# Kernel optimization log

Hardware: AMD Instinct MI355X
Metric: run time of the kernel (lower is better)

## Reference

```python
import jax, jax.numpy as jnp
import numpy as np

INSIZE = 1024
OUTSIZE = 1024
N_U = 20
N_V = 20
SIGMA_MIN = 0.6
SIGMA_MAX = 1.0
R = (SIGMA_MAX - SIGMA_MIN) / 2.0
SIGMA_MEAN = SIGMA_MIN + R
BATCH = 32768


def setup_inputs() -> dict:
    key = jax.random.key(0)
    k_x, k_U, k_p, k_V = jax.random.split(key, 4)
    x = jax.random.normal(k_x, (BATCH, INSIZE), dtype=jnp.float32)
    U = jnp.triu(jax.random.normal(k_U, (INSIZE, INSIZE), dtype=jnp.float32))
    V = jnp.triu(jax.random.normal(k_V, (OUTSIZE, OUTSIZE), dtype=jnp.float32))
    nsigma = min(INSIZE, OUTSIZE)
    p = 0.001 * jax.random.normal(k_p, (nsigma,), dtype=jnp.float32)
    bias = jnp.zeros((OUTSIZE,), dtype=jnp.float32)
    return {"x": x, "U": U, "p": p, "V": V, "bias": bias}


def _hprod(x, u, k):
    # x: [bs, dim], u: [dim], k static int. Householder reflection on the trailing k coords.
    xs = x[:, -k:]                     # [bs, k]
    us = u[-k:]                        # [k]
    alpha = 2.0 * (xs @ us) / jnp.sum(us * us)   # [bs]
    xs_new = xs - alpha[:, None] * us[None, :]
    if k < x.shape[1]:
        return jnp.concatenate([x[:, :-k], xs_new], axis=1)
    return xs_new


def _sigma_matrix(p):
    sigmas = 2.0 * R * (jax.nn.sigmoid(p) - 0.5) + SIGMA_MEAN   # [nsigma]
    nsigma = p.shape[0]
    S = jnp.zeros((INSIZE, OUTSIZE), dtype=p.dtype)
    idx = jnp.arange(nsigma)
    return S.at[idx, idx].set(sigmas)


def reference(x, U, p, V, bias):
    # U multiply: reflectors 0..N_U-1 with k = insize - i
    for i in range(N_U):
        x = _hprod(x, U[i], INSIZE - i)
    x = x @ _sigma_matrix(p)
    # V multiply: reflectors N_V-1..0 with k = outsize - i
    for i in range(N_V - 1, -1, -1):
        x = _hprod(x, V[i], OUTSIZE - i)
    return x + bias
```

## Files before the change

### kernel.cpp

```cpp
#include <hip/hip_runtime.h>
#include <hip/hip_bf16.h>

typedef __attribute__((ext_vector_type(8))) short bf16x8;
typedef __attribute__((ext_vector_type(4))) short bf16x4;
typedef __attribute__((ext_vector_type(4))) float f32x4;

#define NU 20

__device__ __forceinline__ float b2f(unsigned short u) {
    union { float f; unsigned v; } x; x.v = ((unsigned)u) << 16; return x.f;
}
__device__ __forceinline__ unsigned short f2b(float f) {
    union { float f; unsigned v; } x; x.f = f;
    unsigned r = x.v + 0x7FFF + ((x.v >> 16) & 1);
    return (unsigned short)(r >> 16);
}


__global__ __launch_bounds__(256) void k_gram(
        const float* __restrict__ U, const float* __restrict__ p,
        const float* __restrict__ V, const float* __restrict__ bias,
        float* __restrict__ GU, float* __restrict__ GV,
        float* __restrict__ s_ws, float* __restrict__ b_ws) {
    const int b = blockIdx.x, T = threadIdx.x;
    if (b >= 420) {
        int t = (b - 420) * 256 + T;
        float pv = p[t];
        s_ws[t] = 0.4f / (1.0f + __expf(-pv)) + 0.6f;
        b_ws[t] = bias[t];
        return;
    }
    const float* M = (b < 210) ? U : V;
    float* Gm = (b < 210) ? GU : GV;
    int i = (b < 210) ? b : b - 210;
    int k = 0;
    while ((k + 1) * (k + 2) / 2 <= i) k++;
    int j = i - k * (k + 1) / 2;
    f32x4 a4 = *(const f32x4*)&M[j * 1024 + T * 4];
    f32x4 b4 = *(const f32x4*)&M[k * 1024 + T * 4];
    float acc = a4[0] * b4[0] + a4[1] * b4[1] + a4[2] * b4[2] + a4[3] * b4[3];
    for (int off = 32; off; off >>= 1) acc += __shfl_down(acc, off, 64);
    __shared__ float part[4];
    if ((T & 63) == 0) part[T >> 6] = acc;
    __syncthreads();
    if (T == 0) {
        float s = part[0] + part[1] + part[2] + part[3];
        Gm[j * 20 + k] = s; Gm[k * 20 + j] = s;
    }
}

__global__ __launch_bounds__(256) void k_recur(
        const float* __restrict__ U, const float* __restrict__ V,
        const float* __restrict__ GUg, const float* __restrict__ GVg,
        const float* __restrict__ s_ws,
        float* __restrict__ A, float* __restrict__ Csc,
        unsigned short* __restrict__ Ft, unsigned short* __restrict__ G) {
    __shared__ float sGU[400], sGV[400];
    const int T = threadIdx.x;
    const int t = blockIdx.x * 256 + T;
    for (int i = T; i < 400; i += 256) { sGU[i] = GUg[i]; sGV[i] = GVg[i]; }
    __syncthreads();
    float sig = s_ws[t];
    float a[NU], c[NU];
    for (int k = 0; k < NU; k++) {
        float w = U[k * 1024 + t];
        for (int j = 0; j < k; j++) w -= a[j] * sGU[j * 20 + k];
        a[k] = (2.0f / sGU[k * 20 + k]) * w;
    }
    for (int k = NU - 1; k >= 0; k--) {
        float w = V[k * 1024 + t];
        for (int j = k + 1; j < NU; j++) w -= c[j] * sGV[j * 20 + k];
        c[k] = (2.0f / sGV[k * 20 + k]) * w;
    }
    for (int k = 0; k < NU; k++) { A[k * 1024 + t] = a[k]; Ft[k * 1024 + t] = f2b(a[k]); }
    for (int b = 0; b < NU; b++) Csc[b * 1024 + t] = sig * c[b];
    for (int k = 2 * NU; k < 64; k++) Ft[k * 1024 + t] = 0;
    for (int k = 0; k < NU; k++) G[t * 64 + k] = f2b(sig * U[k * 1024 + t]);
    for (int k = 0; k < NU; k++) G[t * 64 + NU + k] = f2b(V[k * 1024 + t]);
    for (int k = 2 * NU; k < 64; k++) G[t * 64 + k] = 0;
}

__global__ __launch_bounds__(256) void k_e(
        const float* __restrict__ U, const float* __restrict__ Csc,
        float* __restrict__ E) {
    const int aa = blockIdx.x / 20, bb = blockIdx.x % 20;
    const int T = threadIdx.x;
    f32x4 a4 = *(const f32x4*)&U[aa * 1024 + T * 4];
    f32x4 b4 = *(const f32x4*)&Csc[bb * 1024 + T * 4];
    float acc = a4[0] * b4[0] + a4[1] * b4[1] + a4[2] * b4[2] + a4[3] * b4[3];
    for (int off = 32; off; off >>= 1) acc += __shfl_down(acc, off, 64);
    __shared__ float part[4];
    if ((T & 63) == 0) part[T >> 6] = acc;
    __syncthreads();
    if (T == 0) E[aa * 20 + bb] = part[0] + part[1] + part[2] + part[3];
}

__global__ __launch_bounds__(256) void k_f2(
        const float* __restrict__ A, const float* __restrict__ Csc,
        const float* __restrict__ Eg, unsigned short* __restrict__ Ft) {
    __shared__ float sE[400];
    const int T = threadIdx.x;
    const int t = blockIdx.x * 256 + T;
    for (int i = T; i < 400; i += 256) sE[i] = Eg[i];
    __syncthreads();
    float av[NU];
    for (int a = 0; a < NU; a++) av[a] = A[a * 1024 + t];
    for (int b = 0; b < NU; b++) {
        float v = Csc[b * 1024 + t];
        for (int a = 0; a < NU; a++) v -= av[a] * sE[a * 20 + b];
        Ft[(NU + b) * 1024 + t] = f2b(v);
    }
}

__global__ __launch_bounds__(256, 4) void k_main(
        const float* __restrict__ x, const unsigned short* __restrict__ Ft,
        const unsigned short* __restrict__ G, const float* __restrict__ s_ws,
        const float* __restrict__ b_ws, float* __restrict__ out) {
    __shared__ __align__(16) float sA[4][16][64];
    __shared__ __align__(16) unsigned short rl[16][72];

    const int T = threadIdx.x;
    const int wv = T >> 6, lane = T & 63;
    const int mc = lane & 15, quad = lane >> 4;
    const int m0 = blockIdx.x * 16;

    f32x4 acc1[4];
#pragma unroll
    for (int i = 0; i < 4; i++) acc1[i] = (f32x4){0.f, 0.f, 0.f, 0.f};

    const float* xp = &x[(size_t)(m0 + mc) * 1024 + wv * 256 + quad * 8];
    const unsigned short* fp = &Ft[(size_t)mc * 1024 + wv * 256 + quad * 8];

    f32x4 xa0 = *(const f32x4*)(xp);
    f32x4 xb0 = *(const f32x4*)(xp + 4);
    f32x4 xa1 = *(const f32x4*)(xp + 32);
    f32x4 xb1 = *(const f32x4*)(xp + 36);
    bf16x8 f0 = *(const bf16x8*)(fp);
    bf16x8 f1 = *(const bf16x8*)(fp + 16384);
    bf16x8 f2 = *(const bf16x8*)(fp + 32768);
    bf16x8 f3 = *(const bf16x8*)(fp + 49152);

#pragma unroll
    for (int ks = 0; ks < 8; ks++) {
        f32x4 xa2, xb2; bf16x8 n0, n1, n2, n3;
        if (ks < 6) {
            const float* xq = xp + (ks + 2) * 32;
            xa2 = *(const f32x4*)(xq);
            xb2 = *(const f32x4*)(xq + 4);
        }
        if (ks < 7) {
            const unsigned short* fq = fp + (ks + 1) * 32;
            n0 = *(const bf16x8*)(fq);
            n1 = *(const bf16x8*)(fq + 16384);
            n2 = *(const bf16x8*)(fq + 32768);
            n3 = *(const bf16x8*)(fq + 49152);
        }
        bf16x8 af;
#pragma unroll
        for (int j = 0; j < 4; j++) {
            af[j]     = (short)f2b(xa0[j]);
            af[j + 4] = (short)f2b(xb0[j]);
        }
        acc1[0] = __builtin_amdgcn_mfma_f32_16x16x32_bf16(af, f0, acc1[0], 0, 0, 0);
        acc1[1] = __builtin_amdgcn_mfma_f32_16x16x32_bf16(af, f1, acc1[1], 0, 0, 0);
        acc1[2] = __builtin_amdgcn_mfma_f32_16x16x32_bf16(af, f2, acc1[2], 0, 0, 0);
        acc1[3] = __builtin_amdgcn_mfma_f32_16x16x32_bf16(af, f3, acc1[3], 0, 0, 0);
        if (ks < 7) {
            xa0 = xa1; xb0 = xb1;
            f0 = n0; f1 = n1; f2 = n2; f3 = n3;
        }
        if (ks < 6) { xa1 = xa2; xb1 = xb2; }
    }

#pragma unroll
    for (int nt = 0; nt < 4; nt++)
#pragma unroll
        for (int rg = 0; rg < 4; rg++)
            sA[wv][quad * 4 + rg][nt * 16 + mc] = acc1[nt][rg];
    __syncthreads();

    {
        const int row = T >> 4, c0 = (T & 15) * 4;
        f32x4 v = *(const f32x4*)&sA[0][row][c0];
#pragma unroll
        for (int w = 1; w < 4; w++) {
            f32x4 u = *(const f32x4*)&sA[w][row][c0];
            v[0] += u[0]; v[1] += u[1]; v[2] += u[2]; v[3] += u[3];
        }
        bf16x4 rv;
#pragma unroll
        for (int j = 0; j < 4; j++) rv[j] = (short)f2b(v[j]);
        *(bf16x4*)&rl[row][c0] = rv;
    }
    __syncthreads();

    bf16x8 pa0 = *(const bf16x8*)&rl[mc][quad * 8];
    bf16x8 pa1 = *(const bf16x8*)&rl[mc][32 + quad * 8];
    const int C0 = wv * 256;

#pragma unroll 2
    for (int nf = 0; nf < 16; nf++) {
        const int col = C0 + nf * 16 + mc;
        const unsigned short* gp = &G[(size_t)col * 64 + quad * 8];
        bf16x8 g0 = *(const bf16x8*)(gp);
        bf16x8 g1 = *(const bf16x8*)(gp + 32);
        f32x4 a = (f32x4){0.f, 0.f, 0.f, 0.f};
        a = __builtin_amdgcn_mfma_f32_16x16x32_bf16(pa0, g0, a, 0, 0, 0);
        a = __builtin_amdgcn_mfma_f32_16x16x32_bf16(pa1, g1, a, 0, 0, 0);
        const float sv = s_ws[col], bv = b_ws[col];
        size_t base = (size_t)(m0 + quad * 4) * 1024 + col;
        out[base]        = x[base]        * sv - a[0] + bv;
        out[base + 1024] = x[base + 1024] * sv - a[1] + bv;
        out[base + 2048] = x[base + 2048] * sv - a[2] + bv;
        out[base + 3072] = x[base + 3072] * sv - a[3] + bv;
    }
}

extern "C" void kernel_launch(void* const* d_in, const int* in_sizes, int n_in,
                              void* d_out, int out_size, void* d_ws, size_t ws_size,
                              hipStream_t stream) {
    const float* x    = (const float*)d_in[0];
    const float* U    = (const float*)d_in[1];
    const float* p    = (const float*)d_in[2];
    const float* V    = (const float*)d_in[3];
    const float* bias = (const float*)d_in[4];

    char* ws = (char*)d_ws;
    unsigned short* Ft = (unsigned short*)ws;
    unsigned short* G  = (unsigned short*)(ws + 131072);
    float* s_ws        = (float*)(ws + 262144);
    float* b_ws        = (float*)(ws + 266240);
    float* GU          = (float*)(ws + 270336);
    float* GV          = (float*)(ws + 274432);
    float* A           = (float*)(ws + 278528);
    float* Csc         = (float*)(ws + 360448);
    float* E           = (float*)(ws + 442368);
    float* out = (float*)d_out;

    hipLaunchKernelGGL(k_gram,  dim3(424),  dim3(256), 0, stream, U, p, V, bias, GU, GV, s_ws, b_ws);
    hipLaunchKernelGGL(k_recur, dim3(4),    dim3(256), 0, stream, U, V, GU, GV, s_ws, A, Csc, Ft, G);
    hipLaunchKernelGGL(k_e,     dim3(400),  dim3(256), 0, stream, U, Csc, E);
    hipLaunchKernelGGL(k_f2,    dim3(4),    dim3(256), 0, stream, A, Csc, E, Ft);
    hipLaunchKernelGGL(k_main,  dim3(2048), dim3(256), 0, stream, x, Ft, G, s_ws, b_ws, out);
}
```

Baseline: 314.4 us.

## Give each wave its own 16 rows with double-buffered direct-to-LDS x staging

k_main now has each wave own a full 16-row tile across all of K instead of splitting K over four waves. That removes the cross-wave shared-memory reduction and its two block barriers. The x tile is streamed through a per-wave double-buffered LDS area using global_load_lds with XOR swizzling and manual vmcnt waits, while Ft fragments are prefetched in registers. Blocks now cover 64 rows, so the grid shrinks to 512 and occupancy drops to 2 blocks per CU. The trade is higher register and LDS use and less parallelism, in exchange for fewer global loads of Ft and better latency hiding.

```diff
diff --git a/kernel.cpp b/kernel.cpp
--- a/kernel.cpp
+++ b/kernel.cpp
@@ -14,6 +14,12 @@
     union { float f; unsigned v; } x; x.f = f;
     unsigned r = x.v + 0x7FFF + ((x.v >> 16) & 1);
     return (unsigned short)(r >> 16);
+}
+
+__device__ __forceinline__ void gload_lds16(const void* g, void* l) {
+    __builtin_amdgcn_global_load_lds(
+        (const __attribute__((address_space(1))) void*)g,
+        (__attribute__((address_space(3))) void*)l, 16, 0, 0);
 }
 
 
@@ -112,95 +118,103 @@
     }
 }
 
-__global__ __launch_bounds__(256, 4) void k_main(
+__global__ __launch_bounds__(256, 2) void k_main(
         const float* __restrict__ x, const unsigned short* __restrict__ Ft,
         const unsigned short* __restrict__ G, const float* __restrict__ s_ws,
         const float* __restrict__ b_ws, float* __restrict__ out) {
-    __shared__ __align__(16) float sA[4][16][64];
-    __shared__ __align__(16) unsigned short rl[16][72];
+    __shared__ __align__(16) float xs[4][2][1024];
+    __shared__ __align__(16) unsigned short rl[4][16][72];
 
     const int T = threadIdx.x;
     const int wv = T >> 6, lane = T & 63;
     const int mc = lane & 15, quad = lane >> 4;
-    const int m0 = blockIdx.x * 16;
+    const int m0 = blockIdx.x * 64 + wv * 16;
+
+#define STAGE(buf, t)                                                           \
+    {                                                                           \
+        _Pragma("unroll")                                                       \
+        for (int i_ = 0; i_ < 4; i_++) {                                        \
+            int r_ = i_ * 4 + (lane >> 4);                                      \
+            int q_ = (lane & 15) ^ r_;                                          \
+            gload_lds16(&x[(size_t)(m0 + r_) * 1024 + (t) * 64 + q_ * 4],       \
+                        &xs[wv][buf][i_ * 256]);                                \
+        }                                                                       \
+    }
 
     f32x4 acc1[4];
 #pragma unroll
     for (int i = 0; i < 4; i++) acc1[i] = (f32x4){0.f, 0.f, 0.f, 0.f};
 
-    const float* xp = &x[(size_t)(m0 + mc) * 1024 + wv * 256 + quad * 8];
-    const unsigned short* fp = &Ft[(size_t)mc * 1024 + wv * 256 + quad * 8];
-
-    f32x4 xa0 = *(const f32x4*)(xp);
-    f32x4 xb0 = *(const f32x4*)(xp + 4);
-    f32x4 xa1 = *(const f32x4*)(xp + 32);
-    f32x4 xb1 = *(const f32x4*)(xp + 36);
-    bf16x8 f0 = *(const bf16x8*)(fp);
-    bf16x8 f1 = *(const bf16x8*)(fp + 16384);
-    bf16x8 f2 = *(const bf16x8*)(fp + 32768);
-    bf16x8 f3 = *(const bf16x8*)(fp + 49152);
-
-#pragma unroll
-    for (int ks = 0; ks < 8; ks++) {
-        f32x4 xa2, xb2; bf16x8 n0, n1, n2, n3;
-        if (ks < 6) {
-            const float* xq = xp + (ks + 2) * 32;
-            xa2 = *(const f32x4*)(xq);
-            xb2 = *(const f32x4*)(xq + 4);
-        }
-        if (ks < 7) {
-            const unsigned short* fq = fp + (ks + 1) * 32;
-            n0 = *(const bf16x8*)(fq);
-            n1 = *(const bf16x8*)(fq + 16384);
-            n2 = *(const bf16x8*)(fq + 32768);
-            n3 = *(const bf16x8*)(fq + 49152);
-        }
-        bf16x8 af;
-#pragma unroll
-        for (int j = 0; j < 4; j++) {
-            af[j]     = (short)f2b(xa0[j]);
-            af[j + 4] = (short)f2b(xb0[j]);
-        }
-        acc1[0] = __builtin_amdgcn_mfma_f32_16x16x32_bf16(af, f0, acc1[0], 0, 0, 0);
-        acc1[1] = __builtin_amdgcn_mfma_f32_16x16x32_bf16(af, f1, acc1[1], 0, 0, 0);
-        acc1[2] = __builtin_amdgcn_mfma_f32_16x16x32_bf16(af, f2, acc1[2], 0, 0, 0);
-        acc1[3] = __builtin_amdgcn_mfma_f32_16x16x32_bf16(af, f3, acc1[3], 0, 0, 0);
-        if (ks < 7) {
-            xa0 = xa1; xb0 = xb1;
-            f0 = n0; f1 = n1; f2 = n2; f3 = n3;
-        }
-        if (ks < 6) { xa1 = xa2; xb1 = xb2; }
-    }
+    const unsigned short* fbase = Ft + (size_t)mc * 1024 + quad * 8;
+    bf16x8 fA[8], fB[8];
+#pragma unroll
+    for (int j = 0; j < 8; j++)
+        fA[j] = *(const bf16x8*)(fbase + (j & 3) * 16384 + (j >> 2) * 32);
+    STAGE(0, 0);
+    STAGE(1, 1);
+
+#pragma unroll
+    for (int t = 0; t < 16; t++) {
+        if (t < 15) asm volatile("s_waitcnt vmcnt(4)" ::: "memory");
+        else        asm volatile("s_waitcnt vmcnt(0)" ::: "memory");
+        __builtin_amdgcn_sched_barrier(0);
+
+        const float* xb = &xs[wv][t & 1][0];
+        bf16x8 af0, af1;
+        {
+            int q0 = quad * 2;
+            f32x4 u0 = *(const f32x4*)&xb[mc * 64 + (q0 ^ mc) * 4];
+            f32x4 u1 = *(const f32x4*)&xb[mc * 64 + ((q0 + 1) ^ mc) * 4];
+#pragma unroll
+            for (int j = 0; j < 4; j++) {
+                af0[j] = (short)f2b(u0[j]);
+                af0[j + 4] = (short)f2b(u1[j]);
+            }
+        }
+        {
+            int q0 = 8 + quad * 2;
+            f32x4 u0 = *(const f32x4*)&xb[mc * 64 + (q0 ^ mc) * 4];
+            f32x4 u1 = *(const f32x4*)&xb[mc * 64 + ((q0 + 1) ^ mc) * 4];
+#pragma unroll
+            for (int j = 0; j < 4; j++) {
+                af1[j] = (short)f2b(u0[j]);
+                af1[j + 4] = (short)f2b(u1[j]);
+            }
+        }
+        acc1[0] = __builtin_amdgcn_mfma_f32_16x16x32_bf16(af0, fA[0], acc1[0], 0, 0, 0);
+        acc1[1] = __builtin_amdgcn_mfma_f32_16x16x32_bf16(af0, fA[1], acc1[1], 0, 0, 0);
+        acc1[2] = __builtin_amdgcn_mfma_f32_16x16x32_bf16(af0, fA[2], acc1[2], 0, 0, 0);
+        acc1[3] = __builtin_amdgcn_mfma_f32_16x16x32_bf16(af0, fA[3], acc1[3], 0, 0, 0);
+        acc1[0] = __builtin_amdgcn_mfma_f32_16x16x32_bf16(af1, fA[4], acc1[0], 0, 0, 0);
+        acc1[1] = __builtin_amdgcn_mfma_f32_16x16x32_bf16(af1, fA[5], acc1[1], 0, 0, 0);
+        acc1[2] = __builtin_amdgcn_mfma_f32_16x16x32_bf16(af1, fA[6], acc1[2], 0, 0, 0);
+        acc1[3] = __builtin_amdgcn_mfma_f32_16x16x32_bf16(af1, fA[7], acc1[3], 0, 0, 0);
+
+        if (t < 15) {
+#pragma unroll
+            for (int j = 0; j < 8; j++)
+                fB[j] = *(const bf16x8*)(fbase + (j & 3) * 16384 + (t + 1) * 64 + (j >> 2) * 32);
+        }
+        __builtin_amdgcn_sched_barrier(0);
+        if (t < 14) STAGE(t & 1, t + 2);
+        if (t < 15) {
+#pragma unroll
+            for (int j = 0; j < 8; j++) fA[j] = fB[j];
+        }
+    }
+#undef STAGE
 
 #pragma unroll
     for (int nt = 0; nt < 4; nt++)
 #pragma unroll
         for (int rg = 0; rg < 4; rg++)
-            sA[wv][quad * 4 + rg][nt * 16 + mc] = acc1[nt][rg];
-    __syncthreads();
-
-    {
-        const int row = T >> 4, c0 = (T & 15) * 4;
-        f32x4 v = *(const f32x4*)&sA[0][row][c0];
-#pragma unroll
-        for (int w = 1; w < 4; w++) {
-            f32x4 u = *(const f32x4*)&sA[w][row][c0];
-            v[0] += u[0]; v[1] += u[1]; v[2] += u[2]; v[3] += u[3];
-        }
-        bf16x4 rv;
-#pragma unroll
-        for (int j = 0; j < 4; j++) rv[j] = (short)f2b(v[j]);
-        *(bf16x4*)&rl[row][c0] = rv;
-    }
-    __syncthreads();
-
-    bf16x8 pa0 = *(const bf16x8*)&rl[mc][quad * 8];
-    bf16x8 pa1 = *(const bf16x8*)&rl[mc][32 + quad * 8];
-    const int C0 = wv * 256;
-
-#pragma unroll 2
-    for (int nf = 0; nf < 16; nf++) {
-        const int col = C0 + nf * 16 + mc;
+            rl[wv][quad * 4 + rg][nt * 16 + mc] = f2b(acc1[nt][rg]);
+    bf16x8 pa0 = *(const bf16x8*)&rl[wv][mc][quad * 8];
+    bf16x8 pa1 = *(const bf16x8*)&rl[wv][mc][32 + quad * 8];
+
+#pragma unroll 4
+    for (int nf = 0; nf < 64; nf++) {
+        const int col = nf * 16 + mc;
         const unsigned short* gp = &G[(size_t)col * 64 + quad * 8];
         bf16x8 g0 = *(const bf16x8*)(gp);
         bf16x8 g1 = *(const bf16x8*)(gp + 32);
@@ -237,9 +251,9 @@
     float* E           = (float*)(ws + 442368);
     float* out = (float*)d_out;
 
-    hipLaunchKernelGGL(k_gram,  dim3(424),  dim3(256), 0, stream, U, p, V, bias, GU, GV, s_ws, b_ws);
-    hipLaunchKernelGGL(k_recur, dim3(4),    dim3(256), 0, stream, U, V, GU, GV, s_ws, A, Csc, Ft, G);
-    hipLaunchKernelGGL(k_e,     dim3(400),  dim3(256), 0, stream, U, Csc, E);
-    hipLaunchKernelGGL(k_f2,    dim3(4),    dim3(256), 0, stream, A, Csc, E, Ft);
-    hipLaunchKernelGGL(k_main,  dim3(2048), dim3(256), 0, stream, x, Ft, G, s_ws, b_ws, out);
-}
+    hipLaunchKernelGGL(k_gram,  dim3(424), dim3(256), 0, stream, U, p, V, bias, GU, GV, s_ws, b_ws);
+    hipLaunchKernelGGL(k_recur, dim3(4),   dim3(256), 0, stream, U, V, GU, GV, s_ws, A, Csc, Ft, G);
+    hipLaunchKernelGGL(k_e,     dim3(400), dim3(256), 0, stream, U, Csc, E);
+    hipLaunchKernelGGL(k_f2,    dim3(4),   dim3(256), 0, stream, A, Csc, E, Ft);
+    hipLaunchKernelGGL(k_main,  dim3(512), dim3(256), 0, stream, x, Ft, G, s_ws, b_ws, out);
+}
```

Measured after the change: 306.2 us. -2.6%, faster.

## Restructure main kernel: LDS-staged x loads, per-wave N split, vectorized epilogue

Applied to the files above, without the earlier changes.

The first GEMM phase now stages x tiles into LDS with global_load_lds, and each wave computes one 16-column slice of the projection over the full K range. This removes the cross-wave reduction through shared memory. The epilogue swaps the MFMA operand order so each lane owns 4 contiguous columns, which allows 16-byte vector loads of x, scale and bias and 16-byte stores. Block-to-tile mapping is swizzled, occupancy is raised to 6 blocks per SM, and the small prep kernels get full unrolling. The cost is more __syncthreads per block and four serialized LDS load phases.

```diff
diff --git a/kernel.cpp b/kernel.cpp
--- a/kernel.cpp
+++ b/kernel.cpp
@@ -14,6 +14,12 @@
     union { float f; unsigned v; } x; x.f = f;
     unsigned r = x.v + 0x7FFF + ((x.v >> 16) & 1);
     return (unsigned short)(r >> 16);
+}
+
+__device__ __forceinline__ void gload_lds16(const void* g, void* l) {
+    __builtin_amdgcn_global_load_lds(
+        (const __attribute__((address_space(1))) void*)g,
+        (__attribute__((address_space(3))) void*)l, 16, 0, 0);
 }
 
 
@@ -62,20 +68,28 @@
     __syncthreads();
     float sig = s_ws[t];
     float a[NU], c[NU];
+#pragma unroll
     for (int k = 0; k < NU; k++) {
         float w = U[k * 1024 + t];
-        for (int j = 0; j < k; j++) w -= a[j] * sGU[j * 20 + k];
+#pragma unroll
+        for (int j = 0; j < NU; j++) if (j < k) w -= a[j] * sGU[j * 20 + k];
         a[k] = (2.0f / sGU[k * 20 + k]) * w;
     }
+#pragma unroll
     for (int k = NU - 1; k >= 0; k--) {
         float w = V[k * 1024 + t];
-        for (int j = k + 1; j < NU; j++) w -= c[j] * sGV[j * 20 + k];
+#pragma unroll
+        for (int j = 0; j < NU; j++) if (j > k) w -= c[j] * sGV[j * 20 + k];
         c[k] = (2.0f / sGV[k * 20 + k]) * w;
     }
+#pragma unroll
     for (int k = 0; k < NU; k++) { A[k * 1024 + t] = a[k]; Ft[k * 1024 + t] = f2b(a[k]); }
+#pragma unroll
     for (int b = 0; b < NU; b++) Csc[b * 1024 + t] = sig * c[b];
     for (int k = 2 * NU; k < 64; k++) Ft[k * 1024 + t] = 0;
+#pragma unroll
     for (int k = 0; k < NU; k++) G[t * 64 + k] = f2b(sig * U[k * 1024 + t]);
+#pragma unroll
     for (int k = 0; k < NU; k++) G[t * 64 + NU + k] = f2b(V[k * 1024 + t]);
     for (int k = 2 * NU; k < 64; k++) G[t * 64 + k] = 0;
 }
@@ -104,115 +118,86 @@
     for (int i = T; i < 400; i += 256) sE[i] = Eg[i];
     __syncthreads();
     float av[NU];
+#pragma unroll
     for (int a = 0; a < NU; a++) av[a] = A[a * 1024 + t];
+#pragma unroll
     for (int b = 0; b < NU; b++) {
         float v = Csc[b * 1024 + t];
+#pragma unroll
         for (int a = 0; a < NU; a++) v -= av[a] * sE[a * 20 + b];
         Ft[(NU + b) * 1024 + t] = f2b(v);
     }
 }
 
-__global__ __launch_bounds__(256, 4) void k_main(
+__global__ __launch_bounds__(256, 6) void k_main(
         const float* __restrict__ x, const unsigned short* __restrict__ Ft,
         const unsigned short* __restrict__ G, const float* __restrict__ s_ws,
         const float* __restrict__ b_ws, float* __restrict__ out) {
-    __shared__ __align__(16) float sA[4][16][64];
+    __shared__ __align__(16) float xs[16][260];
     __shared__ __align__(16) unsigned short rl[16][72];
 
     const int T = threadIdx.x;
     const int wv = T >> 6, lane = T & 63;
     const int mc = lane & 15, quad = lane >> 4;
-    const int m0 = blockIdx.x * 16;
-
-    f32x4 acc1[4];
-#pragma unroll
-    for (int i = 0; i < 4; i++) acc1[i] = (f32x4){0.f, 0.f, 0.f, 0.f};
-
-    const float* xp = &x[(size_t)(m0 + mc) * 1024 + wv * 256 + quad * 8];
-    const unsigned short* fp = &Ft[(size_t)mc * 1024 + wv * 256 + quad * 8];
-
-    f32x4 xa0 = *(const f32x4*)(xp);
-    f32x4 xb0 = *(const f32x4*)(xp + 4);
-    f32x4 xa1 = *(const f32x4*)(xp + 32);
-    f32x4 xb1 = *(const f32x4*)(xp + 36);
-    bf16x8 f0 = *(const bf16x8*)(fp);
-    bf16x8 f1 = *(const bf16x8*)(fp + 16384);
-    bf16x8 f2 = *(const bf16x8*)(fp + 32768);
-    bf16x8 f3 = *(const bf16x8*)(fp + 49152);
-
-#pragma unroll
-    for (int ks = 0; ks < 8; ks++) {
-        f32x4 xa2, xb2; bf16x8 n0, n1, n2, n3;
-        if (ks < 6) {
-            const float* xq = xp + (ks + 2) * 32;
-            xa2 = *(const f32x4*)(xq);
-            xb2 = *(const f32x4*)(xq + 4);
+    const int tile = (blockIdx.x & 7) * 256 + (blockIdx.x >> 3);
+    const int m0 = tile * 16;
+
+    f32x4 acc1 = (f32x4){0.f, 0.f, 0.f, 0.f};
+    const unsigned short* fbase = Ft + (size_t)(wv * 16 + mc) * 1024 + quad * 8;
+
+    for (int t = 0; t < 4; t++) {
+        if (t) __syncthreads();
+#pragma unroll
+        for (int i = 0; i < 4; i++) {
+            int row = wv * 4 + i;
+            gload_lds16(&x[(size_t)(m0 + row) * 1024 + t * 256 + lane * 4], &xs[row][0]);
         }
-        if (ks < 7) {
-            const unsigned short* fq = fp + (ks + 1) * 32;
-            n0 = *(const bf16x8*)(fq);
-            n1 = *(const bf16x8*)(fq + 16384);
-            n2 = *(const bf16x8*)(fq + 32768);
-            n3 = *(const bf16x8*)(fq + 49152);
+        bf16x8 ff[8];
+#pragma unroll
+        for (int kk = 0; kk < 8; kk++)
+            ff[kk] = *(const bf16x8*)(fbase + t * 256 + kk * 32);
+        __syncthreads();
+#pragma unroll
+        for (int kk = 0; kk < 8; kk++) {
+            f32x4 u0 = *(const f32x4*)&xs[mc][kk * 32 + quad * 8];
+            f32x4 u1 = *(const f32x4*)&xs[mc][kk * 32 + quad * 8 + 4];
+            bf16x8 af;
+#pragma unroll
+            for (int j = 0; j < 4; j++) {
+                af[j]     = (short)f2b(u0[j]);
+                af[j + 4] = (short)f2b(u1[j]);
+            }
+            acc1 = __builtin_amdgcn_mfma_f32_16x16x32_bf16(af, ff[kk], acc1, 0, 0, 0);
         }
-        bf16x8 af;
-#pragma unroll
-        for (int j = 0; j < 4; j++) {
-            af[j]     = (short)f2b(xa0[j]);
-            af[j + 4] = (short)f2b(xb0[j]);
-        }
-        acc1[0] = __builtin_amdgcn_mfma_f32_16x16x32_bf16(af, f0, acc1[0], 0, 0, 0);
-        acc1[1] = __builtin_amdgcn_mfma_f32_16x16x32_bf16(af, f1, acc1[1], 0, 0, 0);
-        acc1[2] = __builtin_amdgcn_mfma_f32_16x16x32_bf16(af, f2, acc1[2], 0, 0, 0);
-        acc1[3] = __builtin_amdgcn_mfma_f32_16x16x32_bf16(af, f3, acc1[3], 0, 0, 0);
-        if (ks < 7) {
-            xa0 = xa1; xb0 = xb1;
-            f0 = n0; f1 = n1; f2 = n2; f3 = n3;
-        }
-        if (ks < 6) { xa1 = xa2; xb1 = xb2; }
-    }
-
-#pragma unroll
-    for (int nt = 0; nt < 4; nt++)
-#pragma unroll
-        for (int rg = 0; rg < 4; rg++)
-            sA[wv][quad * 4 + rg][nt * 16 + mc] = acc1[nt][rg];
-    __syncthreads();
-
-    {
-        const int row = T >> 4, c0 = (T & 15) * 4;
-        f32x4 v = *(const f32x4*)&sA[0][row][c0];
-#pragma unroll
-        for (int w = 1; w < 4; w++) {
-            f32x4 u = *(const f32x4*)&sA[w][row][c0];
-            v[0] += u[0]; v[1] += u[1]; v[2] += u[2]; v[3] += u[3];
-        }
-        bf16x4 rv;
-#pragma unroll
-        for (int j = 0; j < 4; j++) rv[j] = (short)f2b(v[j]);
-        *(bf16x4*)&rl[row][c0] = rv;
-    }
+    }
+
+#pragma unroll
+    for (int rg = 0; rg < 4; rg++)
+        rl[quad * 4 + rg][wv * 16 + mc] = f2b(acc1[rg]);
     __syncthreads();
 
     bf16x8 pa0 = *(const bf16x8*)&rl[mc][quad * 8];
     bf16x8 pa1 = *(const bf16x8*)&rl[mc][32 + quad * 8];
+
     const int C0 = wv * 256;
-
 #pragma unroll 2
     for (int nf = 0; nf < 16; nf++) {
-        const int col = C0 + nf * 16 + mc;
-        const unsigned short* gp = &G[(size_t)col * 64 + quad * 8];
+        const int col0 = C0 + nf * 16;
+        const unsigned short* gp = &G[(size_t)(col0 + mc) * 64 + quad * 8];
         bf16x8 g0 = *(const bf16x8*)(gp);
         bf16x8 g1 = *(const bf16x8*)(gp + 32);
         f32x4 a = (f32x4){0.f, 0.f, 0.f, 0.f};
-        a = __builtin_amdgcn_mfma_f32_16x16x32_bf16(pa0, g0, a, 0, 0, 0);
-        a = __builtin_amdgcn_mfma_f32_16x16x32_bf16(pa1, g1, a, 0, 0, 0);
-        const float sv = s_ws[col], bv = b_ws[col];
-        size_t base = (size_t)(m0 + quad * 4) * 1024 + col;
-        out[base]        = x[base]        * sv - a[0] + bv;
-        out[base + 1024] = x[base + 1024] * sv - a[1] + bv;
-        out[base + 2048] = x[base + 2048] * sv - a[2] + bv;
-        out[base + 3072] = x[base + 3072] * sv - a[3] + bv;
+        a = __builtin_amdgcn_mfma_f32_16x16x32_bf16(g0, pa0, a, 0, 0, 0);
+        a = __builtin_amdgcn_mfma_f32_16x16x32_bf16(g1, pa1, a, 0, 0, 0);
+        const int cc = col0 + quad * 4;
+        f32x4 sv = *(const f32x4*)&s_ws[cc];
+        f32x4 bv = *(const f32x4*)&b_ws[cc];
+        size_t base = (size_t)(m0 + mc) * 1024 + cc;
+        f32x4 xv = *(const f32x4*)&x[base];
+        f32x4 o;
+#pragma unroll
+        for (int j = 0; j < 4; j++) o[j] = xv[j] * sv[j] - a[j] + bv[j];
+        *(f32x4*)&out[base] = o;
     }
 }
 
```

After: 299.4 us. -4.8%, faster.
